# Optimization experiments

Measured on AMD Instinct MI355X. Metric: run time of the kernel, lower is better.

The kernel has to match this reference:

```python
import jax, jax.numpy as jnp
import numpy as np


def _ste_round(r):
    # straight-through round
    return r + jax.lax.stop_gradient(jnp.round(r) - r)


def quant_sym(x, s, qn, qp):
    # symmetric LSQ-style fake-quant: clamp(round(x/s)) * s
    r = jnp.clip(x / s, qn, qp)
    return _ste_round(r) * s


def quant_asym(x, s, beta, qn, qp):
    # asymmetric fake-quant with learnable zero-point beta
    r = jnp.clip((x - beta) / s, qn, qp)
    return _ste_round(r) * s + beta


def quant_weight_statsq(w, n_bits=8):
    # statsq: per-output-channel scale from weight statistics
    qp = 2 ** (n_bits - 1) - 1          # 127
    qn = -(2 ** (n_bits - 1))           # -128
    s = 2.0 * jnp.mean(jnp.abs(w), axis=1, keepdims=True) / jnp.sqrt(float(qp))
    return quant_sym(w, s, qn, qp)


def setup_inputs() -> dict:
    key = jax.random.key(0)
    ks = jax.random.split(key, 8)
    B, N, C, H = 4, 4096, 1024, 4096
    x = jax.random.normal(ks[0], (B, N, C), dtype=jnp.float32)
    w1 = jax.random.normal(ks[1], (H, C), dtype=jnp.float32) * (1.0 / np.sqrt(C))
    b1 = jax.random.normal(ks[2], (H,), dtype=jnp.float32) * 0.01
    w2 = jax.random.normal(ks[3], (C, H), dtype=jnp.float32) * (1.0 / np.sqrt(H))
    b2 = jax.random.normal(ks[4], (C,), dtype=jnp.float32) * 0.01
    # learnable LSQ activation scales (per input channel), kept positive
    s_a1 = 0.05 + 0.05 * jax.random.uniform(ks[5], (C,), dtype=jnp.float32)
    s_a2 = 0.02 + 0.02 * jax.random.uniform(ks[6], (H,), dtype=jnp.float32)
    beta2 = jnp.zeros((H,), dtype=jnp.float32)
    return {"x": x, "w1": w1, "b1": b1, "w2": w2, "b2": b2,
            "s_a1": s_a1, "s_a2": s_a2, "beta2": beta2}


def reference(x, w1, b1, w2, b2, s_a1, s_a2, beta2):
    # fc1: symmetric 8-bit LSQ on input, statsq 8-bit on weight
    xq = quant_sym(x, s_a1, -128, 127)
    wq1 = quant_weight_statsq(w1)
    h = jnp.einsum('bnc,hc->bnh', xq, wq1) + b1
    h = jax.nn.gelu(h, approximate=False)  # nn.GELU default (exact erf)
    # drop1 = identity in eval
    # fc2: asymmetric 8-bit LSQ on (non-negative-skewed) activations
    hq = quant_asym(h, s_a2, beta2, 0, 255)
    wq2 = quant_weight_statsq(w2)
    out = jnp.einsum('bnh,ch->bnc', hq, wq2) + b2
    # drop2 = identity in eval
    return out
```

## Files before the change

kernel.cpp:

```cpp
#include <hip/hip_runtime.h>
#include <cstdint>
#include <cstddef>

typedef __attribute__((ext_vector_type(8))) short short8;
typedef __attribute__((ext_vector_type(4))) float f32x4;
typedef __attribute__((ext_vector_type(4))) unsigned short ushort4_t;

__device__ __forceinline__ unsigned short f2bf(float f) {
  unsigned u = __float_as_uint(f);
  u += 0x7FFFu + ((u >> 16) & 1u);
  return (unsigned short)(u >> 16);
}

__device__ __forceinline__ void gload_lds16(const void* g, void* lds) {
  __builtin_amdgcn_global_load_lds((const __attribute__((address_space(1))) void*)g,
                                   (__attribute__((address_space(3))) void*)lds,
                                   16, 0, 0);
}

__device__ __forceinline__ float erf_fast(float v) {
  float x = fabsf(v);
  float t = __builtin_amdgcn_rcpf(fmaf(0.3275911f, x, 1.0f));
  float p = fmaf(1.061405429f, t, -1.453152027f);
  p = fmaf(p, t, 1.421413741f);
  p = fmaf(p, t, -0.284496736f);
  p = fmaf(p, t, 0.254829592f);
  p = p * t;
  float e = fmaf(-p, __expf(-x * x), 1.0f);
  unsigned s = __float_as_uint(v) & 0x80000000u;
  return __uint_as_float(__float_as_uint(e) | s);
}

__device__ __forceinline__ void statsq_row(const float* __restrict__ wr,
                                           unsigned short* __restrict__ wqr, int cols) {
  const int tid = threadIdx.x;
  const float4* w4 = (const float4*)wr;
  const int c4 = cols >> 2;
  float part = 0.f;
  for (int j = tid; j < c4; j += 256) {
    float4 v = w4[j];
    part += fabsf(v.x) + fabsf(v.y) + fabsf(v.z) + fabsf(v.w);
  }
#pragma unroll
  for (int o = 32; o > 0; o >>= 1) part += __shfl_down(part, o, 64);
  __shared__ float wsum[4];
  if ((tid & 63) == 0) wsum[tid >> 6] = part;
  __syncthreads();
  float mean = (wsum[0] + wsum[1] + wsum[2] + wsum[3]) / (float)cols;
  float s = 2.f * mean / sqrtf(127.f);
  ushort4_t* wq4 = (ushort4_t*)wqr;
  for (int j = tid; j < c4; j += 256) {
    float4 v = w4[j];
    float vv[4] = {v.x, v.y, v.z, v.w};
    ushort4_t o;
#pragma unroll
    for (int k = 0; k < 4; ++k) {
      float r = vv[k] / s;
      r = fminf(fmaxf(r, -128.f), 127.f);
      o[k] = f2bf(rintf(r) * s);
    }
    wq4[j] = o;
  }
}

__global__ void quant_fused_kernel(const float* __restrict__ w1, unsigned short* __restrict__ wq1, int C,
                                   const float* __restrict__ w2, unsigned short* __restrict__ wq2, int H,
                                   const float4* __restrict__ x, const float* __restrict__ s_a1,
                                   ushort4_t* __restrict__ xq, int n4, int c4mask) {
  const int NW1 = 4096, NW2 = 1024;
  const int bid = blockIdx.x;
  if (bid < NW1) {
    statsq_row(w1 + (size_t)bid * C, wq1 + (size_t)bid * C, C);
    return;
  }
  if (bid < NW1 + NW2) {
    const int row = bid - NW1;
    statsq_row(w2 + (size_t)row * H, wq2 + (size_t)row * H, H);
    return;
  }
  const int xb = bid - (NW1 + NW2);
  const int nxb = gridDim.x - (NW1 + NW2);
  const int stride = nxb * blockDim.x;
  for (int i = xb * blockDim.x + threadIdx.x; i < n4; i += stride) {
    float4 v = x[i];
    int c = (i & c4mask) << 2;
    float vv[4] = {v.x, v.y, v.z, v.w};
    ushort4_t o;
#pragma unroll
    for (int j = 0; j < 4; ++j) {
      float s = s_a1[c + j];
      float r = vv[j] / s;
      r = fminf(fmaxf(r, -128.f), 127.f);
      o[j] = f2bf(rintf(r) * s);
    }
    xq[i] = o;
  }
}

#define BAR() { asm volatile("" ::: "memory"); __builtin_amdgcn_s_barrier(); asm volatile("" ::: "memory"); }
#define SB() __builtin_amdgcn_sched_barrier(0)
#define LGKM(n) { asm volatile("s_waitcnt lgkmcnt(" #n ")" ::: "memory"); SB(); }
#define VMC(n) { asm volatile("s_waitcnt vmcnt(" #n ")" ::: "memory"); SB(); }
#define PRIO1() __builtin_amdgcn_s_setprio(1)
#define PRIO0() __builtin_amdgcn_s_setprio(0)

#define STG(gbase, ldsbuf, h, kt) { \
  _Pragma("unroll") for (int i_ = 0; i_ < 2; ++i_) { \
    const int rb_ = (h) * 128 + (w * 2 + i_) * 8; \
    gload_lds16((gbase) + (size_t)rb_ * K + (size_t)(kt) * 64, (void*)((ldsbuf) + rb_ * 64)); } }

#define LDA_(dst, buf, mh) { \
  _Pragma("unroll") for (int mi_ = 0; mi_ < 4; ++mi_) { \
    dst[mi_][0] = *(const short8*)((buf) + aBase + (mh) * 4096 + mi_ * 1024 + ck0); \
    dst[mi_][1] = *(const short8*)((buf) + aBase + (mh) * 4096 + mi_ * 1024 + ck1); } }

#define LDBX(dst, buf, base) { \
  _Pragma("unroll") for (int ni_ = 0; ni_ < 2; ++ni_) { \
    dst[ni_][0] = *(const short8*)((buf) + (base) + ni_ * 1024 + ck0); \
    dst[ni_][1] = *(const short8*)((buf) + (base) + ni_ * 1024 + ck1); } }

#define MMQ(aR, bR, mh, nh) { \
  _Pragma("unroll") for (int kk_ = 0; kk_ < 2; ++kk_) \
  _Pragma("unroll") for (int mi_ = 0; mi_ < 4; ++mi_) \
  _Pragma("unroll") for (int ni_ = 0; ni_ < 2; ++ni_) \
    acc[(mh) * 4 + mi_][(nh) * 2 + ni_] = __builtin_amdgcn_mfma_f32_16x16x32_bf16( \
        aR[mi_][kk_], bR[ni_][kk_], acc[(mh) * 4 + mi_][(nh) * 2 + ni_], 0, 0, 0); }

template <int EPI>
__global__ __launch_bounds__(512, 2) void gemm_bt_dc(
    const unsigned short* __restrict__ A, const unsigned short* __restrict__ B,
    const float* __restrict__ bias, const float* __restrict__ s2,
    const float* __restrict__ beta, unsigned short* __restrict__ Cq,
    float* __restrict__ Cf, int N, int K)
{
  __shared__ __align__(16) unsigned short As0[256 * 64];
  __shared__ __align__(16) unsigned short As1[256 * 64];
  __shared__ __align__(16) unsigned short Bs0[256 * 64];
  __shared__ __align__(16) unsigned short Bs1[256 * 64];

  const int tid = threadIdx.x;
  const int w = tid >> 6, ll = tid & 63;
  const int wr = w >> 2, wc = w & 3;

  const int nwg = gridDim.x * gridDim.y;
  const int bid = blockIdx.x + gridDim.x * blockIdx.y;
  const int cpx = nwg >> 3;
  const int swz = (bid & 7) * cpx + (bid >> 3);
  const int gy = gridDim.y;
  const int bx = swz / gy, by = swz - bx * gy;
  const long bm = (long)bx * 256;
  const long bn = (long)by * 256;

  const int srow = ll >> 3;
  const int scol = ((ll & 7) ^ srow) << 3;
  const unsigned short* Agl = A + ((size_t)bm + srow) * K + scol;
  const unsigned short* Bgl = B + ((size_t)bn + srow) * K + scol;

  const int lhi = ll >> 4, llo = ll & 15, l7 = ll & 7;
  const int ck0 = ((0 * 4 + lhi) ^ l7) * 8;
  const int ck1 = ((1 * 4 + lhi) ^ l7) * 8;
  const int aBase = (wr * 128 + llo) * 64;
  const int bBase0 = (wc * 32 + llo) * 64;
  const int bBase1 = (128 + wc * 32 + llo) * 64;

  f32x4 acc[8][4] = {};
  short8 a0[4][2], a1[4][2], b0[2][2], b1[2][2];

  const int nkt = K >> 6;

  STG(Bgl, Bs0, 0, 0); STG(Agl, As0, 0, 0); STG(Agl, As0, 1, 0); STG(Bgl, Bs0, 1, 0);
  STG(Bgl, Bs1, 0, 1); STG(Agl, As1, 0, 1); STG(Agl, As1, 1, 1); STG(Bgl, Bs1, 1, 1);
  VMC(8);
  BAR();
  LDBX(b0, Bs0, bBase0); SB();
  LDA_(a0, As0, 0); SB();

  for (int t = 0; t < nkt; ++t) {
    unsigned short* Asb = (t & 1) ? As1 : As0;
    unsigned short* Bsb = (t & 1) ? Bs1 : Bs0;
    unsigned short* Asn = (t & 1) ? As0 : As1;
    unsigned short* Bsn = (t & 1) ? Bs0 : Bs1;
    const bool i1 = (t + 1 < nkt), i2 = (t + 2 < nkt);

    LDA_(a1, Asb, 1); SB();
    LDBX(b1, Bsb, bBase1); SB();
    LGKM(12);
    PRIO1(); MMQ(a0, b0, 0, 0); PRIO0();

    LGKM(4);
    PRIO1(); MMQ(a1, b0, 1, 0); PRIO0();

    LGKM(0); VMC(0); BAR();
    if (i2) { STG(Agl, Asb, 0, t + 2); STG(Agl, Asb, 1, t + 2); }
    if (i1) { LDBX(b0, Bsn, bBase0); SB(); }
    PRIO1(); MMQ(a0, b1, 0, 1); PRIO0();

    if (i2) { STG(Bgl, Bsb, 0, t + 2); STG(Bgl, Bsb, 1, t + 2); }
    if (i1) { LDA_(a0, Asn, 0); SB(); }
    PRIO1(); MMQ(a1, b1, 1, 1); PRIO0();
  }

  const int lr = lhi;
  const int lc = llo;
#pragma unroll
  for (int NI = 0; NI < 4; ++NI) {
    const long col = bn + wc * 32 + ((NI >= 2) ? 128 : 0) + (NI & 1) * 16 + lc;
    const float bv = bias[col];
    float sv = 1.f, bev = 0.f, inv = 1.f;
    if (EPI == 0) { sv = s2[col]; bev = beta[col]; inv = 1.0f / sv; }
#pragma unroll
    for (int MI = 0; MI < 8; ++MI) {
#pragma unroll
      for (int r = 0; r < 4; ++r) {
        const size_t rowg = (size_t)(bm + wr * 128 + MI * 16 + lr * 4 + r);
        float v = acc[MI][NI][r] + bv;
        if (EPI == 0) {
          float g = 0.5f * v * (1.f + erf_fast(v * 0.70710678118654752f));
          float rr = (g - bev) * inv;
          rr = fminf(fmaxf(rr, 0.f), 255.f);
          Cq[rowg * N + col] = f2bf(fmaf(rintf(rr), sv, bev));
        } else {
          Cf[rowg * N + col] = v;
        }
      }
    }
  }
}

extern "C" void kernel_launch(void* const* d_in, const int* in_sizes, int n_in,
                              void* d_out, int out_size, void* d_ws, size_t ws_size,
                              hipStream_t stream) {
  const float* x     = (const float*)d_in[0];
  const float* w1    = (const float*)d_in[1];
  const float* b1    = (const float*)d_in[2];
  const float* w2    = (const float*)d_in[3];
  const float* b2    = (const float*)d_in[4];
  const float* s_a1  = (const float*)d_in[5];
  const float* s_a2  = (const float*)d_in[6];
  const float* beta2 = (const float*)d_in[7];
  float* out = (float*)d_out;

  const int C = 1024, H = 4096;
  const int M = in_sizes[0] / C;

  unsigned short* xq  = (unsigned short*)d_ws;
  unsigned short* wq1 = xq  + (size_t)M * C;
  unsigned short* wq2 = wq1 + (size_t)H * C;
  unsigned short* hq  = wq2 + (size_t)C * H;

  quant_fused_kernel<<<4096 + 1024 + 2048, 256, 0, stream>>>(
      w1, wq1, C, w2, wq2, H,
      (const float4*)x, s_a1, (ushort4_t*)xq, M * C / 4, C / 4 - 1);

  dim3 g1(M / 256, H / 256);
  gemm_bt_dc<0><<<g1, 512, 0, stream>>>(xq, wq1, b1, s_a2, beta2, hq, nullptr, H, C);
  dim3 g2(M / 256, C / 256);
  gemm_bt_dc<1><<<g2, 512, 0, stream>>>(hq, wq2, b2, nullptr, nullptr, nullptr, out, C, H);
}
```

Baseline: 318.6 us.

## Switch GEMMs to 128x256 tiles with K=32 triple-buffered LDS pipeline

Replaces the 256x256, K=64 double-buffered GEMM with a 128x256 tile, K-step of 32, and a three-stage LDS ring buffer with prefetch distance of two. Launch bounds move to four waves-per-EU occupancy, and the XOR swizzle and fragment addressing are reworked for the narrower K slices. The intent is more resident workgroups and deeper load/compute overlap to hide global-load latency. The costs are lower arithmetic intensity per tile, twice as many loop iterations and barriers, and the 128-VGPR cap needed for four-wave occupancy.

New measurement: 362.6 us. 1.14x slower.

```diff
diff --git a/kernel.cpp b/kernel.cpp
--- a/kernel.cpp
+++ b/kernel.cpp
@@ -12,7 +12,7 @@
   return (unsigned short)(u >> 16);
 }
 
-__device__ __forceinline__ void gload_lds16(const void* g, void* lds) {
+__device__ __forceinline__ void gload_lds16(const void* g, const void* lds) {
   __builtin_amdgcn_global_load_lds((const __attribute__((address_space(1))) void*)g,
                                    (__attribute__((address_space(3))) void*)lds,
                                    16, 0, 0);
@@ -69,10 +69,7 @@
                                    ushort4_t* __restrict__ xq, int n4, int c4mask) {
   const int NW1 = 4096, NW2 = 1024;
   const int bid = blockIdx.x;
-  if (bid < NW1) {
-    statsq_row(w1 + (size_t)bid * C, wq1 + (size_t)bid * C, C);
-    return;
-  }
+  if (bid < NW1) { statsq_row(w1 + (size_t)bid * C, wq1 + (size_t)bid * C, C); return; }
   if (bid < NW1 + NW2) {
     const int row = bid - NW1;
     statsq_row(w2 + (size_t)row * H, wq2 + (size_t)row * H, H);
@@ -104,39 +101,27 @@
 #define PRIO1() __builtin_amdgcn_s_setprio(1)
 #define PRIO0() __builtin_amdgcn_s_setprio(0)
 
-#define STG(gbase, ldsbuf, h, kt) { \
-  _Pragma("unroll") for (int i_ = 0; i_ < 2; ++i_) { \
-    const int rb_ = (h) * 128 + (w * 2 + i_) * 8; \
-    gload_lds16((gbase) + (size_t)rb_ * K + (size_t)(kt) * 64, (void*)((ldsbuf) + rb_ * 64)); } }
-
-#define LDA_(dst, buf, mh) { \
-  _Pragma("unroll") for (int mi_ = 0; mi_ < 4; ++mi_) { \
-    dst[mi_][0] = *(const short8*)((buf) + aBase + (mh) * 4096 + mi_ * 1024 + ck0); \
-    dst[mi_][1] = *(const short8*)((buf) + aBase + (mh) * 4096 + mi_ * 1024 + ck1); } }
-
-#define LDBX(dst, buf, base) { \
-  _Pragma("unroll") for (int ni_ = 0; ni_ < 2; ++ni_) { \
-    dst[ni_][0] = *(const short8*)((buf) + (base) + ni_ * 1024 + ck0); \
-    dst[ni_][1] = *(const short8*)((buf) + (base) + ni_ * 1024 + ck1); } }
-
-#define MMQ(aR, bR, mh, nh) { \
-  _Pragma("unroll") for (int kk_ = 0; kk_ < 2; ++kk_) \
-  _Pragma("unroll") for (int mi_ = 0; mi_ < 4; ++mi_) \
-  _Pragma("unroll") for (int ni_ = 0; ni_ < 2; ++ni_) \
-    acc[(mh) * 4 + mi_][(nh) * 2 + ni_] = __builtin_amdgcn_mfma_f32_16x16x32_bf16( \
-        aR[mi_][kk_], bR[ni_][kk_], acc[(mh) * 4 + mi_][(nh) * 2 + ni_], 0, 0, 0); }
+#define RD(p) (*(const short8*)(p))
+
+#define STG3(kt, OFF) { \
+  gload_lds16(Ags + (size_t)(kt) * 32, (const void*)(lds + (OFF) + w * 512)); \
+  gload_lds16(Bgs0 + (size_t)(kt) * 32, (const void*)(lds + (OFF) + 4096 + w * 512)); \
+  gload_lds16(Bgs1 + (size_t)(kt) * 32, (const void*)(lds + (OFF) + 8192 + w * 512)); }
+
+#define MMQ4(aF, bF, mh, nh) { \
+  _Pragma("unroll") for (int i_ = 0; i_ < 2; ++i_) \
+  _Pragma("unroll") for (int j_ = 0; j_ < 2; ++j_) \
+    acc[(mh) * 2 + i_][(nh) * 2 + j_] = __builtin_amdgcn_mfma_f32_16x16x32_bf16( \
+        aF[i_], bF[j_], acc[(mh) * 2 + i_][(nh) * 2 + j_], 0, 0, 0); }
 
 template <int EPI>
-__global__ __launch_bounds__(512, 2) void gemm_bt_dc(
+__global__ __launch_bounds__(512, 4) void gemm_bt_hp(
     const unsigned short* __restrict__ A, const unsigned short* __restrict__ B,
     const float* __restrict__ bias, const float* __restrict__ s2,
     const float* __restrict__ beta, unsigned short* __restrict__ Cq,
     float* __restrict__ Cf, int N, int K)
 {
-  __shared__ __align__(16) unsigned short As0[256 * 64];
-  __shared__ __align__(16) unsigned short As1[256 * 64];
-  __shared__ __align__(16) unsigned short Bs0[256 * 64];
-  __shared__ __align__(16) unsigned short Bs1[256 * 64];
+  __shared__ __align__(16) unsigned short lds[3 * 12288];
 
   const int tid = threadIdx.x;
   const int w = tid >> 6, ll = tid & 63;
@@ -148,71 +133,71 @@
   const int swz = (bid & 7) * cpx + (bid >> 3);
   const int gy = gridDim.y;
   const int bx = swz / gy, by = swz - bx * gy;
-  const long bm = (long)bx * 256;
+  const long bm = (long)bx * 128;
   const long bn = (long)by * 256;
 
-  const int srow = ll >> 3;
-  const int scol = ((ll & 7) ^ srow) << 3;
-  const unsigned short* Agl = A + ((size_t)bm + srow) * K + scol;
-  const unsigned short* Bgl = B + ((size_t)bn + srow) * K + scol;
-
-  const int lhi = ll >> 4, llo = ll & 15, l7 = ll & 7;
-  const int ck0 = ((0 * 4 + lhi) ^ l7) * 8;
-  const int ck1 = ((1 * 4 + lhi) ^ l7) * 8;
-  const int aBase = (wr * 128 + llo) * 64;
-  const int bBase0 = (wc * 32 + llo) * 64;
-  const int bBase1 = (128 + wc * 32 + llo) * 64;
-
-  f32x4 acc[8][4] = {};
-  short8 a0[4][2], a1[4][2], b0[2][2], b1[2][2];
-
-  const int nkt = K >> 6;
-
-  STG(Bgl, Bs0, 0, 0); STG(Agl, As0, 0, 0); STG(Agl, As0, 1, 0); STG(Bgl, Bs0, 1, 0);
-  STG(Bgl, Bs1, 0, 1); STG(Agl, As1, 0, 1); STG(Agl, As1, 1, 1); STG(Bgl, Bs1, 1, 1);
-  VMC(8);
+  const int ra = tid >> 2;
+  const int ga = (tid & 3) ^ ((tid >> 3) & 3);
+  const unsigned short* Ags  = A + ((size_t)bm + ra) * K + ga * 8;
+  const unsigned short* Bgs0 = B + ((size_t)bn + ra) * K + ga * 8;
+  const unsigned short* Bgs1 = B + ((size_t)bn + 128 + ra) * K + ga * 8;
+
+  const int llo = ll & 15, lhi = ll >> 4;
+  const int gread = lhi ^ ((llo >> 1) & 3);
+  const unsigned short* aP = lds + ((wr * 64 + llo) * 32 + gread * 8);
+  const unsigned short* bP = lds + (4096 + (wc * 64 + llo) * 32 + gread * 8);
+
+  f32x4 acc[4][4] = {};
+  short8 a0[2], a1[2], b0[2], b1[2];
+
+  const int nkt = K >> 5;
+
+  STG3(0, 0); STG3(1, 12288); STG3(2, 24576);
+  VMC(6);
   BAR();
-  LDBX(b0, Bs0, bBase0); SB();
-  LDA_(a0, As0, 0); SB();
-
+  b0[0] = RD(bP + 0);   b0[1] = RD(bP + 512);  SB();
+  a0[0] = RD(aP + 0);   a0[1] = RD(aP + 512);  SB();
+
+  int curOff = 0, nxtOff = 12288;
   for (int t = 0; t < nkt; ++t) {
-    unsigned short* Asb = (t & 1) ? As1 : As0;
-    unsigned short* Bsb = (t & 1) ? Bs1 : Bs0;
-    unsigned short* Asn = (t & 1) ? As0 : As1;
-    unsigned short* Bsn = (t & 1) ? Bs0 : Bs1;
-    const bool i1 = (t + 1 < nkt), i2 = (t + 2 < nkt);
-
-    LDA_(a1, Asb, 1); SB();
-    LDBX(b1, Bsb, bBase1); SB();
-    LGKM(12);
-    PRIO1(); MMQ(a0, b0, 0, 0); PRIO0();
-
+    const bool i1 = (t + 1 < nkt), i2 = (t + 2 < nkt), i3 = (t + 3 < nkt);
+
+    a1[0] = RD(aP + curOff + 1024); a1[1] = RD(aP + curOff + 1536); SB();
+    b1[0] = RD(bP + curOff + 1024); b1[1] = RD(bP + curOff + 1536); SB();
     LGKM(4);
-    PRIO1(); MMQ(a1, b0, 1, 0); PRIO0();
-
-    LGKM(0); VMC(0); BAR();
-    if (i2) { STG(Agl, Asb, 0, t + 2); STG(Agl, Asb, 1, t + 2); }
-    if (i1) { LDBX(b0, Bsn, bBase0); SB(); }
-    PRIO1(); MMQ(a0, b1, 0, 1); PRIO0();
-
-    if (i2) { STG(Bgl, Bsb, 0, t + 2); STG(Bgl, Bsb, 1, t + 2); }
-    if (i1) { LDA_(a0, Asn, 0); SB(); }
-    PRIO1(); MMQ(a1, b1, 1, 1); PRIO0();
+    PRIO1(); MMQ4(a0, b0, 0, 0); PRIO0();
+
+    LGKM(2);
+    PRIO1(); MMQ4(a1, b0, 1, 0); PRIO0();
+
+    LGKM(0);
+    if (i2)      { VMC(3); }
+    else if (i1) { VMC(0); }
+    BAR();
+    if (i3) STG3(t + 3, curOff);
+    if (i1) { b0[0] = RD(bP + nxtOff); b0[1] = RD(bP + nxtOff + 512); SB(); }
+    PRIO1(); MMQ4(a0, b1, 0, 1); PRIO0();
+
+    if (i1) { a0[0] = RD(aP + nxtOff); a0[1] = RD(aP + nxtOff + 512); SB(); }
+    PRIO1(); MMQ4(a1, b1, 1, 1); PRIO0();
+
+    curOff = nxtOff;
+    nxtOff = (nxtOff == 24576) ? 0 : nxtOff + 12288;
   }
 
   const int lr = lhi;
   const int lc = llo;
 #pragma unroll
   for (int NI = 0; NI < 4; ++NI) {
-    const long col = bn + wc * 32 + ((NI >= 2) ? 128 : 0) + (NI & 1) * 16 + lc;
+    const long col = bn + wc * 64 + NI * 16 + lc;
     const float bv = bias[col];
     float sv = 1.f, bev = 0.f, inv = 1.f;
     if (EPI == 0) { sv = s2[col]; bev = beta[col]; inv = 1.0f / sv; }
 #pragma unroll
-    for (int MI = 0; MI < 8; ++MI) {
+    for (int MI = 0; MI < 4; ++MI) {
 #pragma unroll
       for (int r = 0; r < 4; ++r) {
-        const size_t rowg = (size_t)(bm + wr * 128 + MI * 16 + lr * 4 + r);
+        const size_t rowg = (size_t)(bm + wr * 64 + MI * 16 + lr * 4 + r);
         float v = acc[MI][NI][r] + bv;
         if (EPI == 0) {
           float g = 0.5f * v * (1.f + erf_fast(v * 0.70710678118654752f));
@@ -252,8 +237,8 @@
       w1, wq1, C, w2, wq2, H,
       (const float4*)x, s_a1, (ushort4_t*)xq, M * C / 4, C / 4 - 1);
 
-  dim3 g1(M / 256, H / 256);
-  gemm_bt_dc<0><<<g1, 512, 0, stream>>>(xq, wq1, b1, s_a2, beta2, hq, nullptr, H, C);
-  dim3 g2(M / 256, C / 256);
-  gemm_bt_dc<1><<<g2, 512, 0, stream>>>(hq, wq2, b2, nullptr, nullptr, nullptr, out, C, H);
-}
+  dim3 g1(M / 128, H / 256);
+  gemm_bt_hp<0><<<g1, 512, 0, stream>>>(xq, wq1, b1, s_a2, beta2, hq, nullptr, H, C);
+  dim3 g2(M / 128, C / 256);
+  gemm_bt_hp<1><<<g2, 512, 0, stream>>>(hq, wq2, b2, nullptr, nullptr, nullptr, out, C, H);
+}
```
